# Performance work log

Measured on AMD Instinct MI355X. Metric: run time of the kernel, lower is better.

Reference implementation:

```python
import jax, jax.numpy as jnp
import numpy as np

E, TOPK, H, I, NSH = 8, 2, 2048, 5120, 2
B, S = 2, 1024


def setup_inputs() -> dict:
    key = jax.random.key(0)
    ks = jax.random.split(key, 8)
    sc = 0.02
    return {
        "x": jax.random.normal(ks[0], (B, S, H), dtype=jnp.float32),
        "w_router": jax.random.normal(ks[1], (E, H), dtype=jnp.float32),
        "wg": jax.random.normal(ks[2], (E, I, H), dtype=jnp.float32) * sc,
        "wu": jax.random.normal(ks[3], (E, I, H), dtype=jnp.float32) * sc,
        "wd": jax.random.normal(ks[4], (E, H, I), dtype=jnp.float32) * sc,
        "sg": jax.random.normal(ks[5], (NSH, I, H), dtype=jnp.float32) * sc,
        "su": jax.random.normal(ks[6], (NSH, I, H), dtype=jnp.float32) * sc,
        "sd": jax.random.normal(ks[7], (NSH, H, I), dtype=jnp.float32) * sc,
    }


def reference(x, w_router, wg, wu, wd, sg, su, sd):
    b, s, h = x.shape
    xt = x.reshape(-1, h)  # [T, H]
    T = xt.shape[0]

    # Router: fp32 linear, sigmoid scores, top-k, renormalize
    logits = jnp.einsum('th,eh->te', xt.astype(jnp.float32), w_router.astype(jnp.float32))
    scores = jax.nn.sigmoid(logits)
    topk_w, topk_i = jax.lax.top_k(scores, TOPK)
    topk_w = topk_w / jnp.sum(topk_w, axis=-1, keepdims=True)

    # Dense combine weights [T, E]: zero for non-selected experts
    comb = jnp.zeros((T, E), dtype=xt.dtype)
    comb = comb.at[jnp.arange(T)[:, None], topk_i].add(topk_w.astype(xt.dtype))

    # Routed experts (SwiGLU, no bias): compute all, combine with sparse weights
    gate = jax.nn.silu(jnp.einsum('th,eih->tei', xt, wg))
    up = jnp.einsum('th,eih->tei', xt, wu)
    expert_out = jnp.einsum('tei,ehi->teh', gate * up, wd)
    out = jnp.einsum('te,teh->th', comb, expert_out)

    # Shared experts: applied to every token, summed
    sgate = jax.nn.silu(jnp.einsum('th,jih->tji', xt, sg))
    sup = jnp.einsum('th,jih->tji', xt, su)
    out = out + jnp.einsum('tji,jhi->th', sgate * sup, sd)

    return out.reshape(b, s, h)
```

## Files before the change

kernel.cpp:

```cpp
#include <hip/hip_runtime.h>
#include <stdint.h>


#define E_ 8
#define H_ 2048
#define I_ 5120
#define T_ 2048
#define NSLOT 10

typedef __attribute__((ext_vector_type(4))) float f32x4;
typedef __attribute__((ext_vector_type(8))) __bf16 bf16x8;
typedef __attribute__((ext_vector_type(4))) unsigned int u32x4;
typedef __attribute__((ext_vector_type(2))) unsigned int u32x2;

__device__ __forceinline__ int sw(int r) { return (r ^ (r >> 2)) & 3; }

__device__ __forceinline__ unsigned short f2bf(float f) {
  unsigned u = __builtin_bit_cast(unsigned, f);
  u += 0x7FFFu + ((u >> 16) & 1u);
  return (unsigned short)(u >> 16);
}

__device__ __forceinline__ u32x2 cvt4(f32x4 v) {
  unsigned r0, r1;
  asm("v_cvt_pk_bf16_f32 %0, %1, %2" : "=v"(r0) : "v"(v[0]), "v"(v[1]));
  asm("v_cvt_pk_bf16_f32 %0, %1, %2" : "=v"(r1) : "v"(v[2]), "v"(v[3]));
  u32x2 w; w[0] = r0; w[1] = r1;
  return w;
}

__global__ __launch_bounds__(256) void k_castx(const float* __restrict__ x,
                                               unsigned short* __restrict__ xb) {
  const int i = (blockIdx.x * 256 + threadIdx.x) * 8;
  f32x4 a = *(const f32x4*)(x + i);
  f32x4 b = *(const f32x4*)(x + i + 4);
  u32x2 lo = cvt4(a), hi = cvt4(b);
  u32x4 o; o[0] = lo[0]; o[1] = lo[1]; o[2] = hi[0]; o[3] = hi[1];
  *(u32x4*)(xb + i) = o;
}

__global__ __launch_bounds__(64) void k_router(const float* __restrict__ x,
                                               const float* __restrict__ wr,
                                               int* __restrict__ tki,
                                               float* __restrict__ tkw) {
  const int t = blockIdx.x, lane = threadIdx.x;
  const float* xr = x + (size_t)t * H_;
  float lg[E_];
#pragma unroll
  for (int e = 0; e < E_; ++e) {
    const float* w = wr + (size_t)e * H_;
    float acc = 0.f;
    for (int k = lane; k < H_; k += 64) acc += xr[k] * w[k];
#pragma unroll
    for (int off = 32; off > 0; off >>= 1) acc += __shfl_down(acc, off);
    lg[e] = acc;
  }
  if (lane == 0) {
    float sc[E_];
#pragma unroll
    for (int e = 0; e < E_; ++e) sc[e] = 1.f / (1.f + expf(-lg[e]));
    int b0 = 0;
#pragma unroll
    for (int e = 1; e < E_; ++e) if (sc[e] > sc[b0]) b0 = e;
    int b1 = -1;
#pragma unroll
    for (int e = 0; e < E_; ++e) {
      if (e == b0) continue;
      if (b1 < 0 || sc[e] > sc[b1]) b1 = e;
    }
    float s0 = sc[b0], s1 = sc[b1], inv = 1.f / (s0 + s1);
    tki[2 * t] = b0; tki[2 * t + 1] = b1;
    tkw[2 * t] = s0 * inv; tkw[2 * t + 1] = s1 * inv;
  }
}

__global__ __launch_bounds__(64) void k_lists(const int* __restrict__ tki,
                                              const float* __restrict__ tkw,
                                              int* __restrict__ elist,
                                              float* __restrict__ ew,
                                              int* __restrict__ ecnt) {
  const int s = blockIdx.x, lane = threadIdx.x;
  if (s < E_) {
    int base = 0;
    for (int c = 0; c < T_ / 64; ++c) {
      int t = c * 64 + lane;
      int i0 = tki[2 * t], i1 = tki[2 * t + 1];
      int flag = (i0 == s) ? 1 : ((i1 == s) ? 2 : 0);
      unsigned long long m = __ballot(flag != 0);
      int pre = __popcll(m & ((1ull << lane) - 1ull));
      if (flag) {
        elist[s * T_ + base + pre] = t;
        ew[s * T_ + base + pre] = tkw[2 * t + flag - 1];
      }
      base += __popcll(m);
    }
    int padded = (base + 255) & ~255;
    for (int p = base + lane; p < padded; p += 64) { elist[s * T_ + p] = 0; ew[s * T_ + p] = 0.f; }
    if (lane == 0) ecnt[s] = base;
  } else {
    for (int i = lane; i < T_; i += 64) { elist[s * T_ + i] = i; ew[s * T_ + i] = 1.f; }
    if (lane == 0) ecnt[s] = T_;
  }
}

__global__ void k_bases(const int* __restrict__ ecnt, int* __restrict__ sbase) {
  if (threadIdx.x == 0 && blockIdx.x == 0) {
    int b = 0;
    for (int s = 0; s < NSLOT; ++s) { sbase[s] = b; b += (ecnt[s] + 255) & ~255; }
  }
}

__global__ __launch_bounds__(1024, 4) void k_gateup(
    const unsigned short* __restrict__ xb,
    const float* __restrict__ wg_all, const float* __restrict__ wu_all,
    const float* __restrict__ sg_all, const float* __restrict__ su_all,
    const int* __restrict__ elist, const float* __restrict__ ew,
    const int* __restrict__ ecnt,
    const int* __restrict__ sbase, unsigned short* __restrict__ h) {
  const int s = blockIdx.z;
  const int cnt = ecnt[s];
  const int r0 = blockIdx.y * 256;
  if (r0 >= cnt) return;
  const int n0 = blockIdx.x * 128;
  const float* gw; const float* uw;
  if (s < E_) { gw = wg_all + (size_t)s * I_ * H_; uw = wu_all + (size_t)s * I_ * H_; }
  else        { gw = sg_all + (size_t)(s - E_) * I_ * H_; uw = su_all + (size_t)(s - E_) * I_ * H_; }
  const int* lst = elist + s * T_;
  const int hrow0 = sbase[s] + r0;

  __shared__ u32x4 sA[2][256 * 4];
  __shared__ u32x4 sG[2][128 * 4];
  __shared__ u32x4 sU[2][128 * 4];

  const int tid = threadIdx.x;
  const int w = tid >> 6, lane = tid & 63;
  const int wr = w >> 2, wc = w & 3;
  const int fr = lane & 15, k8 = lane >> 4;

  const int ar = tid >> 2, ca = tid & 3;
  int li = r0 + ar; if (li >= cnt) li = r0;
  const unsigned short* xp = xb + (size_t)lst[li] * H_ + ca * 8;
  const int br = tid >> 3, cb = (tid & 7) >> 1, bh = tid & 1;
  const float* gp = gw + (size_t)(n0 + br) * H_ + (tid & 7) * 4;
  const float* up = uw + (size_t)(n0 + br) * H_ + (tid & 7) * 4;

  u32x4 ra; f32x4 rg, ru;

  f32x4 accg[4][2], accu[4][2];
#pragma unroll
  for (int m = 0; m < 4; ++m)
#pragma unroll
    for (int n = 0; n < 2; ++n) {
      accg[m][n] = (f32x4){0.f, 0.f, 0.f, 0.f};
      accu[m][n] = (f32x4){0.f, 0.f, 0.f, 0.f};
    }

  auto loadNext = [&]() {
    ra = *(const u32x4*)xp; rg = *(const f32x4*)gp; ru = *(const f32x4*)up;
    xp += 32; gp += 32; up += 32;
  };
  auto stage = [&](int b) {
    sA[b][ar * 4 + (ca ^ sw(ar))] = ra;
    ((u32x2*)&sG[b][br * 4 + (cb ^ sw(br))])[bh] = cvt4(rg);
    ((u32x2*)&sU[b][br * 4 + (cb ^ sw(br))])[bh] = cvt4(ru);
  };
  auto compute = [&](int b) {
    bf16x8 af[4], gf[2], uf[2];
#pragma unroll
    for (int m = 0; m < 4; ++m) {
      int r = wr * 64 + m * 16 + fr;
      af[m] = __builtin_bit_cast(bf16x8, sA[b][r * 4 + (k8 ^ sw(r))]);
    }
#pragma unroll
    for (int n = 0; n < 2; ++n) {
      int r = wc * 32 + n * 16 + fr;
      gf[n] = __builtin_bit_cast(bf16x8, sG[b][r * 4 + (k8 ^ sw(r))]);
      uf[n] = __builtin_bit_cast(bf16x8, sU[b][r * 4 + (k8 ^ sw(r))]);
    }
#pragma unroll
    for (int m = 0; m < 4; ++m)
#pragma unroll
      for (int n = 0; n < 2; ++n) {
        accg[m][n] = __builtin_amdgcn_mfma_f32_16x16x32_bf16(af[m], gf[n], accg[m][n], 0, 0, 0);
        accu[m][n] = __builtin_amdgcn_mfma_f32_16x16x32_bf16(af[m], uf[n], accu[m][n], 0, 0, 0);
      }
  };

  const int KT = H_ / 32;
  loadNext();
  stage(0);
  loadNext();
  __syncthreads();
  int cur = 0;
  for (int kt = 0; kt < KT; ++kt) {
    compute(cur);
    if (kt + 1 < KT) {
      stage(cur ^ 1);
      if (kt + 2 < KT) loadNext();
      __syncthreads();
      cur ^= 1;
    }
  }

#pragma unroll
  for (int m = 0; m < 4; ++m)
#pragma unroll
    for (int r = 0; r < 4; ++r) {
      int rit = wr * 64 + m * 16 + k8 * 4 + r;
      if (r0 + rit < cnt) {
        float wgt = ew[s * T_ + r0 + rit];
        unsigned short* hrow = h + (size_t)(hrow0 + rit) * I_ + n0 + wc * 32;
#pragma unroll
        for (int n = 0; n < 2; ++n) {
          float g = accg[m][n][r], uv = accu[m][n][r];
          float hv = g / (1.f + expf(-g)) * uv * wgt;
          hrow[n * 16 + fr] = f2bf(hv);
        }
      }
    }
}

#define KSPLIT 4
__global__ __launch_bounds__(512, 4) void k_down(
    const unsigned short* __restrict__ h,
    const float* __restrict__ wd_all, const float* __restrict__ sd_all,
    const int* __restrict__ elist,
    const int* __restrict__ ecnt, const int* __restrict__ sbase,
    float* __restrict__ out) {
  const int s = blockIdx.z;
  const int cnt = ecnt[s];
  const int r0 = blockIdx.y * 256;
  if (r0 >= cnt) return;
  const int nt = blockIdx.x & 15;
  const int ks = blockIdx.x >> 4;
  const int n0 = nt * 128;
  const int kbase = ks * (I_ / KSPLIT);
  const float* bw = (s < E_) ? wd_all + (size_t)s * H_ * I_
                             : sd_all + (size_t)(s - E_) * H_ * I_;
  const int hrow0 = sbase[s] + r0;

  __shared__ u32x4 sA[2][256 * 4];
  __shared__ u32x4 sB[2][128 * 4];

  const int tid = threadIdx.x;
  const int wv = tid >> 6, lane = tid & 63;
  const int wr = wv >> 1, wc = wv & 1;
  const int fr = lane & 15, k8 = lane >> 4;

  const int ar = tid >> 1, ca2 = (tid & 1) * 2;
  const unsigned short* hp = h + (size_t)(hrow0 + ar) * I_ + kbase + ca2 * 8;
  const int brr = tid >> 2, cb = tid & 3;
  const float* bp = bw + (size_t)(n0 + brr) * I_ + kbase + cb * 8;

  u32x4 ra0, ra1; f32x4 rb0, rb1;

  f32x4 acc[4][4];
#pragma unroll
  for (int m = 0; m < 4; ++m)
#pragma unroll
    for (int n = 0; n < 4; ++n) acc[m][n] = (f32x4){0.f, 0.f, 0.f, 0.f};

  auto loadNext = [&]() {
    ra0 = *(const u32x4*)hp; ra1 = *(const u32x4*)(hp + 8); hp += 32;
    rb0 = *(const f32x4*)bp; rb1 = *(const f32x4*)(bp + 4); bp += 32;
  };
  auto stage = [&](int b) {
    sA[b][ar * 4 + (ca2 ^ sw(ar))] = ra0;
    sA[b][ar * 4 + ((ca2 + 1) ^ sw(ar))] = ra1;
    u32x2 lo = cvt4(rb0), hi = cvt4(rb1);
    u32x4 q; q[0] = lo[0]; q[1] = lo[1]; q[2] = hi[0]; q[3] = hi[1];
    sB[b][brr * 4 + (cb ^ sw(brr))] = q;
  };
  auto compute = [&](int b) {
    bf16x8 af[4], bf[4];
#pragma unroll
    for (int m = 0; m < 4; ++m) {
      int r = wr * 64 + m * 16 + fr;
      af[m] = __builtin_bit_cast(bf16x8, sA[b][r * 4 + (k8 ^ sw(r))]);
    }
#pragma unroll
    for (int n = 0; n < 4; ++n) {
      int r = wc * 64 + n * 16 + fr;
      bf[n] = __builtin_bit_cast(bf16x8, sB[b][r * 4 + (k8 ^ sw(r))]);
    }
#pragma unroll
    for (int m = 0; m < 4; ++m)
#pragma unroll
      for (int n = 0; n < 4; ++n)
        acc[m][n] = __builtin_amdgcn_mfma_f32_16x16x32_bf16(af[m], bf[n], acc[m][n], 0, 0, 0);
  };

  const int KT = I_ / 32 / KSPLIT;
  loadNext();
  stage(0);
  loadNext();
  __syncthreads();
  int cur = 0;
  for (int kt = 0; kt < KT; ++kt) {
    compute(cur);
    if (kt + 1 < KT) {
      stage(cur ^ 1);
      if (kt + 2 < KT) loadNext();
      __syncthreads();
      cur ^= 1;
    }
  }

  const int* lst = elist + s * T_;
#pragma unroll
  for (int m = 0; m < 4; ++m)
#pragma unroll
    for (int r = 0; r < 4; ++r) {
      int rit = wr * 64 + m * 16 + k8 * 4 + r;
      if (r0 + rit < cnt) {
        int t = lst[r0 + rit];
        float* orow = out + (size_t)t * H_ + n0 + wc * 64 + fr;
#pragma unroll
        for (int n = 0; n < 4; ++n) atomicAdd(orow + n * 16, acc[m][n][r]);
      }
    }
}

extern "C" void kernel_launch(void* const* d_in, const int* in_sizes, int n_in,
                              void* d_out, int out_size, void* d_ws, size_t ws_size,
                              hipStream_t stream) {
  const float* x  = (const float*)d_in[0];
  const float* wr = (const float*)d_in[1];
  const float* wg = (const float*)d_in[2];
  const float* wu = (const float*)d_in[3];
  const float* wd = (const float*)d_in[4];
  const float* sg = (const float*)d_in[5];
  const float* su = (const float*)d_in[6];
  const float* sd = (const float*)d_in[7];
  float* out = (float*)d_out;
  char* ws = (char*)d_ws;

  int*   tki   = (int*)(ws);
  float* tkw   = (float*)(ws + 16384);
  int*   elist = (int*)(ws + 32768);
  float* ew    = (float*)(ws + 114688);
  int*   ecnt  = (int*)(ws + 196608);
  int*   sbase = (int*)(ws + 196864);
  unsigned short* xb = (unsigned short*)(ws + 262144);
  unsigned short* h  = (unsigned short*)(ws + 262144 + 8388608);

  k_castx<<<T_ * H_ / (256 * 8), 256, 0, stream>>>(x, xb);
  k_router<<<T_, 64, 0, stream>>>(x, wr, tki, tkw);
  k_lists<<<NSLOT, 64, 0, stream>>>(tki, tkw, elist, ew, ecnt);
  k_bases<<<1, 1, 0, stream>>>(ecnt, sbase);
  k_gateup<<<dim3(I_ / 128, T_ / 256, NSLOT), 1024, 0, stream>>>(
      xb, wg, wu, sg, su, elist, ew, ecnt, sbase, h);
  hipMemsetAsync(out, 0, (size_t)T_ * H_ * sizeof(float), stream);
  k_down<<<dim3((H_ / 128) * KSPLIT, T_ / 256, NSLOT), 512, 0, stream>>>(
      h, wd, sd, elist, ecnt, sbase, out);
}
```

Baseline: 1.0000 ms.

## Drop split-K in down projection and replace atomics with a gather-combine kernel

The down-projection GEMM no longer splits K four ways. Each block now runs the full I dimension and writes its per-slot result rows densely into a workspace buffer `y`. A new `k_combine` kernel then sums, for each token, its two routed-expert rows and two shared-expert rows, using positions recorded by `k_lists`. This removes the large volume of fp32 atomicAdds to the output and the memset of `out`. The costs are an extra round trip to memory through `y`, a grid four times smaller with longer K loops per block, and a large workspace requirement; if the workspace is too small it falls back to the atomic path, still without split-K.

```diff
diff --git a/kernel.cpp b/kernel.cpp
--- a/kernel.cpp
+++ b/kernel.cpp
@@ -78,7 +78,8 @@
                                               const float* __restrict__ tkw,
                                               int* __restrict__ elist,
                                               float* __restrict__ ew,
-                                              int* __restrict__ ecnt) {
+                                              int* __restrict__ ecnt,
+                                              int* __restrict__ ipos) {
   const int s = blockIdx.x, lane = threadIdx.x;
   if (s < E_) {
     int base = 0;
@@ -91,6 +92,7 @@
       if (flag) {
         elist[s * T_ + base + pre] = t;
         ew[s * T_ + base + pre] = tkw[2 * t + flag - 1];
+        ipos[2 * t + flag - 1] = base + pre;
       }
       base += __popcll(m);
     }
@@ -220,21 +222,18 @@
     }
 }
 
-#define KSPLIT 4
 __global__ __launch_bounds__(512, 4) void k_down(
     const unsigned short* __restrict__ h,
     const float* __restrict__ wd_all, const float* __restrict__ sd_all,
     const int* __restrict__ elist,
     const int* __restrict__ ecnt, const int* __restrict__ sbase,
+    float* __restrict__ y, int use_y,
     float* __restrict__ out) {
   const int s = blockIdx.z;
   const int cnt = ecnt[s];
   const int r0 = blockIdx.y * 256;
   if (r0 >= cnt) return;
-  const int nt = blockIdx.x & 15;
-  const int ks = blockIdx.x >> 4;
-  const int n0 = nt * 128;
-  const int kbase = ks * (I_ / KSPLIT);
+  const int n0 = blockIdx.x * 128;
   const float* bw = (s < E_) ? wd_all + (size_t)s * H_ * I_
                              : sd_all + (size_t)(s - E_) * H_ * I_;
   const int hrow0 = sbase[s] + r0;
@@ -248,9 +247,9 @@
   const int fr = lane & 15, k8 = lane >> 4;
 
   const int ar = tid >> 1, ca2 = (tid & 1) * 2;
-  const unsigned short* hp = h + (size_t)(hrow0 + ar) * I_ + kbase + ca2 * 8;
+  const unsigned short* hp = h + (size_t)(hrow0 + ar) * I_ + ca2 * 8;
   const int brr = tid >> 2, cb = tid & 3;
-  const float* bp = bw + (size_t)(n0 + brr) * I_ + kbase + cb * 8;
+  const float* bp = bw + (size_t)(n0 + brr) * I_ + cb * 8;
 
   u32x4 ra0, ra1; f32x4 rb0, rb1;
 
@@ -290,7 +289,7 @@
         acc[m][n] = __builtin_amdgcn_mfma_f32_16x16x32_bf16(af[m], bf[n], acc[m][n], 0, 0, 0);
   };
 
-  const int KT = I_ / 32 / KSPLIT;
+  const int KT = I_ / 32;
   loadNext();
   stage(0);
   loadNext();
@@ -306,19 +305,52 @@
     }
   }
 
-  const int* lst = elist + s * T_;
-#pragma unroll
-  for (int m = 0; m < 4; ++m)
-#pragma unroll
-    for (int r = 0; r < 4; ++r) {
-      int rit = wr * 64 + m * 16 + k8 * 4 + r;
-      if (r0 + rit < cnt) {
-        int t = lst[r0 + rit];
-        float* orow = out + (size_t)t * H_ + n0 + wc * 64 + fr;
-#pragma unroll
-        for (int n = 0; n < 4; ++n) atomicAdd(orow + n * 16, acc[m][n][r]);
-      }
-    }
+  if (use_y) {
+#pragma unroll
+    for (int m = 0; m < 4; ++m)
+#pragma unroll
+      for (int r = 0; r < 4; ++r) {
+        int rit = wr * 64 + m * 16 + k8 * 4 + r;
+        float* yrow = y + (size_t)(hrow0 + rit) * H_ + n0 + wc * 64 + fr;
+#pragma unroll
+        for (int n = 0; n < 4; ++n) yrow[n * 16] = acc[m][n][r];
+      }
+  } else {
+    const int* lst = elist + s * T_;
+#pragma unroll
+    for (int m = 0; m < 4; ++m)
+#pragma unroll
+      for (int r = 0; r < 4; ++r) {
+        int rit = wr * 64 + m * 16 + k8 * 4 + r;
+        if (r0 + rit < cnt) {
+          int t = lst[r0 + rit];
+          float* orow = out + (size_t)t * H_ + n0 + wc * 64 + fr;
+#pragma unroll
+          for (int n = 0; n < 4; ++n) atomicAdd(orow + n * 16, acc[m][n][r]);
+        }
+      }
+  }
+}
+
+__global__ __launch_bounds__(256) void k_combine(
+    const float* __restrict__ y, const int* __restrict__ tki,
+    const int* __restrict__ ipos, const int* __restrict__ sbase,
+    float* __restrict__ out) {
+  const int t = blockIdx.x;
+  const int c = threadIdx.x * 8;
+  const size_t r0 = (size_t)(sbase[tki[2 * t]] + ipos[2 * t]) * H_ + c;
+  const size_t r1 = (size_t)(sbase[tki[2 * t + 1]] + ipos[2 * t + 1]) * H_ + c;
+  const size_t r2 = (size_t)(sbase[8] + t) * H_ + c;
+  const size_t r3 = (size_t)(sbase[9] + t) * H_ + c;
+  f32x4 a0 = *(const f32x4*)(y + r0), b0 = *(const f32x4*)(y + r0 + 4);
+  f32x4 a1 = *(const f32x4*)(y + r1), b1 = *(const f32x4*)(y + r1 + 4);
+  f32x4 a2 = *(const f32x4*)(y + r2), b2 = *(const f32x4*)(y + r2 + 4);
+  f32x4 a3 = *(const f32x4*)(y + r3), b3 = *(const f32x4*)(y + r3 + 4);
+  f32x4 sa = (a0 + a1) + (a2 + a3);
+  f32x4 sb = (b0 + b1) + (b2 + b3);
+  float* o = out + (size_t)t * H_ + c;
+  *(f32x4*)o = sa;
+  *(f32x4*)(o + 4) = sb;
 }
 
 extern "C" void kernel_launch(void* const* d_in, const int* in_sizes, int n_in,
@@ -341,16 +373,22 @@
   float* ew    = (float*)(ws + 114688);
   int*   ecnt  = (int*)(ws + 196608);
   int*   sbase = (int*)(ws + 196864);
+  int*   ipos  = (int*)(ws + 197632);
   unsigned short* xb = (unsigned short*)(ws + 262144);
   unsigned short* h  = (unsigned short*)(ws + 262144 + 8388608);
+  float* y = (float*)(ws + 262144 + 8388608 + 107479040);
+  const size_t ws_need_y = 262144ull + 8388608ull + 107479040ull + 85983232ull;
+  const int use_y = (ws_size >= ws_need_y) ? 1 : 0;
 
   k_castx<<<T_ * H_ / (256 * 8), 256, 0, stream>>>(x, xb);
   k_router<<<T_, 64, 0, stream>>>(x, wr, tki, tkw);
-  k_lists<<<NSLOT, 64, 0, stream>>>(tki, tkw, elist, ew, ecnt);
+  k_lists<<<NSLOT, 64, 0, stream>>>(tki, tkw, elist, ew, ecnt, ipos);
   k_bases<<<1, 1, 0, stream>>>(ecnt, sbase);
   k_gateup<<<dim3(I_ / 128, T_ / 256, NSLOT), 1024, 0, stream>>>(
       xb, wg, wu, sg, su, elist, ew, ecnt, sbase, h);
-  hipMemsetAsync(out, 0, (size_t)T_ * H_ * sizeof(float), stream);
-  k_down<<<dim3((H_ / 128) * KSPLIT, T_ / 256, NSLOT), 512, 0, stream>>>(
-      h, wd, sd, elist, ecnt, sbase, out);
-}
+  if (!use_y) hipMemsetAsync(out, 0, (size_t)T_ * H_ * sizeof(float), stream);
+  k_down<<<dim3(H_ / 128, T_ / 256, NSLOT), 512, 0, stream>>>(
+      h, wd, sd, elist, ecnt, sbase, y, use_y, out);
+  if (use_y)
+    k_combine<<<T_, 256, 0, stream>>>(y, tki, ipos, sbase, out);
+}
```

New measurement: 998.7 us. About the same (-0.1%).
